# Kernel tuning notes

Hardware: AMD Instinct MI355X
Metric: run time of the kernel (lower is better)

## Reference

```python
import jax, jax.numpy as jnp
import numpy as np
from jax import lax

BIG = 1e30  # finite stand-in for +inf to keep grads NaN-free


def _iso_inc(y):
    """Exact non-decreasing isotonic regression (L2) of a 1-D vector via the
    minimax formula: v_i = max_{j<=i} min_{k>=i} mean(y[j..k]).
    Vectorized O(n^2); equivalent to PAVA."""
    n = y.shape[0]
    csum = jnp.concatenate([jnp.zeros((1,), y.dtype), jnp.cumsum(y)])
    j = jnp.arange(n)[:, None]   # row index (block start)
    k = jnp.arange(n)[None, :]   # col index (block end / position i)
    valid = k >= j
    denom = jnp.where(valid, k - j + 1, 1).astype(y.dtype)
    mean = jnp.where(valid, (csum[k + 1] - csum[j]) / denom, BIG)  # [n, n]
    # A[j, i] = min_{k >= i} mean[j, k]
    A = lax.cummin(mean, axis=1, reverse=True)
    # v_i = max_{j <= i} A[j, i]
    B = jnp.where(j <= k, A, -BIG)
    return jnp.max(B, axis=0)


def _iso_dec(y):
    """Non-increasing isotonic regression (what torchsort's isotonic_l2 solves)."""
    return -_iso_inc(-y)


def _soft_rank_l2(x, strength):
    """torchsort.soft_rank with regularization='l2' (Blondel et al. 2020).
    x: [b, n]; rank along last dim. r = s - iso_dec(s - w) un-permuted,
    where s = sort(x/strength, descending) and w = [n, n-1, ..., 1]."""
    n = x.shape[-1]
    theta = x / strength
    perm = jnp.argsort(-theta, axis=-1)                 # descending sort order
    s = jnp.take_along_axis(theta, perm, axis=-1)
    w = jnp.arange(n, 0, -1).astype(x.dtype)            # [n, n-1, ..., 1]
    iso = jax.vmap(_iso_dec)(s - w)
    ret_sorted = s - iso
    inv = jnp.argsort(perm, axis=-1)                    # inverse permutation
    return jnp.take_along_axis(ret_sorted, inv, axis=-1)


def setup_inputs() -> dict:
    key = jax.random.key(0)
    k1, k2 = jax.random.split(key)
    pred = jax.random.normal(k1, (8, 2048), dtype=jnp.float32)
    target = jax.random.normal(k2, (8, 2048), dtype=jnp.float32)
    return {"pred": pred, "target": target}


def reference(pred, target):
    reg_strength = 1.0
    pred_rank = _soft_rank_l2(pred, reg_strength)
    target_rank = _soft_rank_l2(target, reg_strength)
    pc = pred_rank - pred_rank.mean(axis=-1, keepdims=True)
    tc = target_rank - target_rank.mean(axis=-1, keepdims=True)
    covariance = (pc * tc).sum(axis=-1)
    pred_std = jnp.sqrt((pc ** 2).sum(axis=-1))
    target_std = jnp.sqrt((tc ** 2).sum(axis=-1))
    spearman = covariance / (pred_std * target_std + 1e-8)
    return 1.0 - jnp.mean(spearman)
```

## Files before the change

### kernel.cpp

```cpp
#include <hip/hip_runtime.h>
#include <math.h>

#define N      2048
#define B      8
#define NROW   16
#define CHUNKS 16
#define EPB    128
#define K1T    512
#define K2T    512
#define HALF   256
#define EPT    8

typedef unsigned long long u64;
typedef unsigned int       u32;

#define WS_CORRD_OFF (NROW * N * sizeof(int))

__device__ inline u32 f2key(float f) {
    u32 u = __float_as_uint(f);
    return (u & 0x80000000u) ? ~u : (u | 0x80000000u);
}
__device__ inline double wave_red(double v) {
#pragma unroll
    for (int o = 32; o > 0; o >>= 1) v += __shfl_down(v, o, 64);
    return v;
}

__global__ __launch_bounds__(K1T) void count_pos_kernel(
        const float* __restrict__ pred, const float* __restrict__ target,
        int* __restrict__ posg) {
    __shared__ u64 keys[N];
    __shared__ u32 scnt[K1T];

    const int t  = threadIdx.x;
    const int rr = blockIdx.x >> 4;
    const int ch = blockIdx.x & 15;
    const float* row = (rr < B) ? pred + (size_t)rr * N
                                : target + (size_t)(rr - B) * N;

    {
        const float4 v = *(const float4*)(row + t * 4);
        const int g = t * 4;
        keys[g + 0] = ((u64)f2key(v.x) << 32) | (u32)(g + 0);
        keys[g + 1] = ((u64)f2key(v.y) << 32) | (u32)(g + 1);
        keys[g + 2] = ((u64)f2key(v.z) << 32) | (u32)(g + 2);
        keys[g + 3] = ((u64)f2key(v.w) << 32) | (u32)(g + 3);
    }
    __syncthreads();
    {
        const int e  = t & (EPB - 1);
        const int h  = t >> 7;
        const u64 Ki = keys[ch * EPB + e];
        u32 cnt = 0;
        const int j0 = h * (N / 4);
#pragma unroll 8
        for (int j = j0; j < j0 + N / 4; ++j)
            cnt += (keys[j] > Ki) ? 1u : 0u;
        scnt[t] = cnt;
    }
    __syncthreads();
    if (t < EPB) {
        const u32 p = scnt[t] + scnt[t + 128] + scnt[t + 256] + scnt[t + 384];
        posg[rr * N + ch * EPB + t] = (int)p;
    }
}

__global__ __launch_bounds__(K2T) void pava_rank_corr_kernel(
        const float* __restrict__ pred, const float* __restrict__ target,
        const int* __restrict__ posg, double* __restrict__ corrd) {
    __shared__ float  sv[2][N];
    __shared__ double bsum[2][N];
    __shared__ int    bcnt[2][N];
    __shared__ int    nb[2][HALF];
    __shared__ int    nf_sh[2];
    __shared__ float  rank[2][N];
    __shared__ double redA[8], redB[8], redC[8], redD[8], redE[8];

    const int t  = threadIdx.x;
    const int r  = t >> 8;
    const int tt = t & (HALF - 1);
    const int b  = blockIdx.x;

    const float* row = (r == 0 ? pred : target) + (size_t)b * N;
    const int*   pos = posg + (size_t)(r == 0 ? b : b + B) * N;

    float v8[EPT]; int p8[EPT];
    {
        const int i0 = tt * EPT;
        const float4 va = *(const float4*)(row + i0);
        const float4 vb = *(const float4*)(row + i0 + 4);
        v8[0]=va.x; v8[1]=va.y; v8[2]=va.z; v8[3]=va.w;
        v8[4]=vb.x; v8[5]=vb.y; v8[6]=vb.z; v8[7]=vb.w;
        const int4 pa = *(const int4*)(pos + i0);
        const int4 pb = *(const int4*)(pos + i0 + 4);
        p8[0]=pa.x; p8[1]=pa.y; p8[2]=pa.z; p8[3]=pa.w;
        p8[4]=pb.x; p8[5]=pb.y; p8[6]=pb.z; p8[7]=pb.w;
#pragma unroll
        for (int e = 0; e < EPT; ++e) sv[r][p8[e]] = v8[e];
    }
    __syncthreads();

    {
        const int base = tt * EPT;
        int m = 0;
#pragma unroll
        for (int e = 0; e < EPT; ++e) {
            const int g = base + e;
            double s = (double)sv[r][g] - (double)(N - g);
            int q = 1;
            while (m > 0) {
                const double ps = bsum[r][base + m - 1];
                const int    pq = bcnt[r][base + m - 1];
                if (ps * (double)q < s * (double)pq) { s += ps; q += pq; --m; }
                else break;
            }
            bsum[r][base + m] = s; bcnt[r][base + m] = q; ++m;
        }
        nb[r][tt] = m;
    }

    for (int l = 0; l < 8; ++l) {
        __syncthreads();
        const int pairs = HALF >> (l + 1);
        if (tt < pairs) {
            const int W  = 1 << l;
            const int c  = tt << (l + 1);
            const int lb = c * EPT;
            const int rb = (c + W) * EPT;
            int m = nb[r][c];
            const int rn = nb[r][c + W];
            for (int x = 0; x < rn; ++x) {
                double s = bsum[r][rb + x]; int q = bcnt[r][rb + x];
                while (m > 0) {
                    const double ps = bsum[r][lb + m - 1];
                    const int    pq = bcnt[r][lb + m - 1];
                    if (ps * (double)q < s * (double)pq) { s += ps; q += pq; --m; }
                    else break;
                }
                bsum[r][lb + m] = s; bcnt[r][lb + m] = q; ++m;
            }
            nb[r][c] = m;
        }
    }
    __syncthreads();

    if (tt == 0) {
        const int m = nb[r][0];
        float* bm = (float*)&bsum[r][0];
        int st = 0;
        for (int f = 0; f < m; ++f) {
            const int    cq = bcnt[r][f];
            const double s  = bsum[r][f];
            bcnt[r][f] = st;
            bm[f] = (float)(s / (double)cq);
            st += cq;
        }
        nf_sh[r] = m;
    }
    __syncthreads();

    {
        const int m = nf_sh[r];
        const float* bm = (const float*)&bsum[r][0];
        const int i0 = tt * EPT;
#pragma unroll
        for (int e = 0; e < EPT; ++e) {
            const int p = p8[e];
            int lo = 0, hi = m - 1;
            while (lo < hi) {
                const int mid = (lo + hi + 1) >> 1;
                if (bcnt[r][mid] <= p) lo = mid; else hi = mid - 1;
            }
            rank[r][i0 + e] = v8[e] - bm[lo];
        }
    }
    __syncthreads();

    double sp = 0, st = 0, spp = 0, stt = 0, spt = 0;
    for (int i = t; i < N; i += K2T) {
        const double a = (double)rank[0][i];
        const double c = (double)rank[1][i];
        sp += a; st += c; spp += a * a; stt += c * c; spt += a * c;
    }
    sp  = wave_red(sp);  st  = wave_red(st);
    spp = wave_red(spp); stt = wave_red(stt); spt = wave_red(spt);
    const int w = t >> 6, lane = t & 63;
    if (lane == 0) { redA[w]=sp; redB[w]=st; redC[w]=spp; redD[w]=stt; redE[w]=spt; }
    __syncthreads();
    if (t == 0) {
        double a=0, c=0, aa=0, cc=0, ac=0;
        for (int i = 0; i < 8; ++i) { a+=redA[i]; c+=redB[i]; aa+=redC[i]; cc+=redD[i]; ac+=redE[i]; }
        const double n   = (double)N;
        const double cv  = ac - a * c / n;
        const double vp2 = aa - a * a / n;
        const double vt2 = cc - c * c / n;
        corrd[b] = cv / (sqrt(vp2) * sqrt(vt2) + 1e-8);
    }
}

__global__ void finalize_kernel(const double* __restrict__ corrd,
                                float* __restrict__ out) {
    if (threadIdx.x == 0 && blockIdx.x == 0) {
        double s = 0.0;
        for (int i = 0; i < B; ++i) s += corrd[i];
        out[0] = (float)(1.0 - s / (double)B);
    }
}

extern "C" void kernel_launch(void* const* d_in, const int* in_sizes, int n_in,
                              void* d_out, int out_size, void* d_ws, size_t ws_size,
                              hipStream_t stream) {
    const float* pred   = (const float*)d_in[0];
    const float* target = (const float*)d_in[1];
    float*  out   = (float*)d_out;
    int*    posg  = (int*)d_ws;
    double* corrd = (double*)((char*)d_ws + WS_CORRD_OFF);

    count_pos_kernel<<<NROW * CHUNKS, K1T, 0, stream>>>(pred, target, posg);
    pava_rank_corr_kernel<<<B, K2T, 0, stream>>>(pred, target, posg, corrd);
    finalize_kernel<<<1, 64, 0, stream>>>(corrd, out);
}
```

Baseline: 26.06 us.

## Scatter sorted values in count kernel and fold finalize into atomic add

The counting kernel now writes each element's value to its sorted position in a global buffer and initializes the output to 1. The PAVA kernel reads the presorted values directly instead of doing a shared-memory scatter plus barrier, and it defers the original value and position loads until after the merges. The correlation reduction keeps the pred ranks in registers, and the separate finalize kernel is replaced by a float atomicAdd, removing one kernel launch. This relies on stream ordering for the output initialization, and float atomics make the final summation order nondeterministic.

```diff
diff --git a/kernel.cpp b/kernel.cpp
--- a/kernel.cpp
+++ b/kernel.cpp
@@ -14,12 +14,17 @@
 typedef unsigned long long u64;
 typedef unsigned int       u32;
 
-#define WS_CORRD_OFF (NROW * N * sizeof(int))
+#define WS_POS 0
+#define WS_SV  (NROW * N)
 
 __device__ inline u32 f2key(float f) {
     u32 u = __float_as_uint(f);
     return (u & 0x80000000u) ? ~u : (u | 0x80000000u);
 }
+__device__ inline float key2f(u32 u) {
+    u = (u & 0x80000000u) ? (u & 0x7fffffffu) : ~u;
+    return __uint_as_float(u);
+}
 __device__ inline double wave_red(double v) {
 #pragma unroll
     for (int o = 32; o > 0; o >>= 1) v += __shfl_down(v, o, 64);
@@ -28,7 +33,8 @@
 
 __global__ __launch_bounds__(K1T) void count_pos_kernel(
         const float* __restrict__ pred, const float* __restrict__ target,
-        int* __restrict__ posg) {
+        int* __restrict__ posg, float* __restrict__ svg,
+        float* __restrict__ out) {
     __shared__ u64 keys[N];
     __shared__ u32 scnt[K1T];
 
@@ -37,6 +43,8 @@
     const int ch = blockIdx.x & 15;
     const float* row = (rr < B) ? pred + (size_t)rr * N
                                 : target + (size_t)(rr - B) * N;
+
+    if (blockIdx.x == 0 && t == 0) out[0] = 1.0f;
 
     {
         const float4 v = *(const float4*)(row + t * 4);
@@ -61,60 +69,48 @@
     __syncthreads();
     if (t < EPB) {
         const u32 p = scnt[t] + scnt[t + 128] + scnt[t + 256] + scnt[t + 384];
+        const u64 Ki = keys[ch * EPB + t];
         posg[rr * N + ch * EPB + t] = (int)p;
+        svg[rr * N + (int)p] = key2f((u32)(Ki >> 32));
     }
 }
 
 __global__ __launch_bounds__(K2T) void pava_rank_corr_kernel(
         const float* __restrict__ pred, const float* __restrict__ target,
-        const int* __restrict__ posg, double* __restrict__ corrd) {
-    __shared__ float  sv[2][N];
+        const int* __restrict__ posg, const float* __restrict__ svg,
+        float* __restrict__ out) {
     __shared__ double bsum[2][N];
     __shared__ int    bcnt[2][N];
     __shared__ int    nb[2][HALF];
     __shared__ int    nf_sh[2];
-    __shared__ float  rank[2][N];
-    __shared__ double redA[8], redB[8], redC[8], redD[8], redE[8];
+    __shared__ float  rankt[N];
+    __shared__ double red[5][4];
 
     const int t  = threadIdx.x;
     const int r  = t >> 8;
     const int tt = t & (HALF - 1);
     const int b  = blockIdx.x;
-
-    const float* row = (r == 0 ? pred : target) + (size_t)b * N;
-    const int*   pos = posg + (size_t)(r == 0 ? b : b + B) * N;
-
-    float v8[EPT]; int p8[EPT];
-    {
-        const int i0 = tt * EPT;
-        const float4 va = *(const float4*)(row + i0);
-        const float4 vb = *(const float4*)(row + i0 + 4);
-        v8[0]=va.x; v8[1]=va.y; v8[2]=va.z; v8[3]=va.w;
-        v8[4]=vb.x; v8[5]=vb.y; v8[6]=vb.z; v8[7]=vb.w;
-        const int4 pa = *(const int4*)(pos + i0);
-        const int4 pb = *(const int4*)(pos + i0 + 4);
-        p8[0]=pa.x; p8[1]=pa.y; p8[2]=pa.z; p8[3]=pa.w;
-        p8[4]=pb.x; p8[5]=pb.y; p8[6]=pb.z; p8[7]=pb.w;
-#pragma unroll
-        for (int e = 0; e < EPT; ++e) sv[r][p8[e]] = v8[e];
-    }
-    __syncthreads();
-
-    {
-        const int base = tt * EPT;
+    const int rowid = (r == 0) ? b : b + B;
+    const int i0 = tt * EPT;
+
+    {
+        const float* svrow = svg + (size_t)rowid * N;
+        const float4 sa = *(const float4*)(svrow + i0);
+        const float4 sb = *(const float4*)(svrow + i0 + 4);
+        const float s8[EPT] = {sa.x, sa.y, sa.z, sa.w, sb.x, sb.y, sb.z, sb.w};
         int m = 0;
 #pragma unroll
         for (int e = 0; e < EPT; ++e) {
-            const int g = base + e;
-            double s = (double)sv[r][g] - (double)(N - g);
+            const int g = i0 + e;
+            double s = (double)s8[e] - (double)(N - g);
             int q = 1;
             while (m > 0) {
-                const double ps = bsum[r][base + m - 1];
-                const int    pq = bcnt[r][base + m - 1];
+                const double ps = bsum[r][i0 + m - 1];
+                const int    pq = bcnt[r][i0 + m - 1];
                 if (ps * (double)q < s * (double)pq) { s += ps; q += pq; --m; }
                 else break;
             }
-            bsum[r][base + m] = s; bcnt[r][base + m] = q; ++m;
+            bsum[r][i0 + m] = s; bcnt[r][i0 + m] = q; ++m;
         }
         nb[r][tt] = m;
     }
@@ -159,10 +155,18 @@
     }
     __syncthreads();
 
-    {
+    float r8[EPT];
+    {
+        const float* row = (r == 0 ? pred : target) + (size_t)b * N;
+        const int*   pos = posg + (size_t)rowid * N;
+        const float4 va = *(const float4*)(row + i0);
+        const float4 vb = *(const float4*)(row + i0 + 4);
+        const float v8[EPT] = {va.x, va.y, va.z, va.w, vb.x, vb.y, vb.z, vb.w};
+        const int4 pa = *(const int4*)(pos + i0);
+        const int4 pb = *(const int4*)(pos + i0 + 4);
+        const int p8[EPT] = {pa.x, pa.y, pa.z, pa.w, pb.x, pb.y, pb.z, pb.w};
         const int m = nf_sh[r];
         const float* bm = (const float*)&bsum[r][0];
-        const int i0 = tt * EPT;
 #pragma unroll
         for (int e = 0; e < EPT; ++e) {
             const int p = p8[e];
@@ -171,39 +175,44 @@
                 const int mid = (lo + hi + 1) >> 1;
                 if (bcnt[r][mid] <= p) lo = mid; else hi = mid - 1;
             }
-            rank[r][i0 + e] = v8[e] - bm[lo];
-        }
-    }
-    __syncthreads();
-
-    double sp = 0, st = 0, spp = 0, stt = 0, spt = 0;
-    for (int i = t; i < N; i += K2T) {
-        const double a = (double)rank[0][i];
-        const double c = (double)rank[1][i];
-        sp += a; st += c; spp += a * a; stt += c * c; spt += a * c;
-    }
-    sp  = wave_red(sp);  st  = wave_red(st);
-    spp = wave_red(spp); stt = wave_red(stt); spt = wave_red(spt);
-    const int w = t >> 6, lane = t & 63;
-    if (lane == 0) { redA[w]=sp; redB[w]=st; redC[w]=spp; redD[w]=stt; redE[w]=spt; }
+            r8[e] = v8[e] - bm[lo];
+        }
+    }
+    if (r == 1) {
+#pragma unroll
+        for (int e = 0; e < EPT; ++e) rankt[i0 + e] = r8[e];
+    }
+    __syncthreads();
+
+    if (r == 0) {
+        double sp = 0, st = 0, spp = 0, stt = 0, spt = 0;
+#pragma unroll
+        for (int e = 0; e < EPT; ++e) {
+            const double a = (double)r8[e];
+            const double c = (double)rankt[i0 + e];
+            sp += a; st += c; spp += a * a; stt += c * c; spt += a * c;
+        }
+        sp  = wave_red(sp);  st  = wave_red(st);
+        spp = wave_red(spp); stt = wave_red(stt); spt = wave_red(spt);
+        const int w = t >> 6, lane = t & 63;
+        if (lane == 0) {
+            red[0][w] = sp; red[1][w] = st; red[2][w] = spp;
+            red[3][w] = stt; red[4][w] = spt;
+        }
+    }
     __syncthreads();
     if (t == 0) {
-        double a=0, c=0, aa=0, cc=0, ac=0;
-        for (int i = 0; i < 8; ++i) { a+=redA[i]; c+=redB[i]; aa+=redC[i]; cc+=redD[i]; ac+=redE[i]; }
+        double a = 0, c = 0, aa = 0, cc = 0, ac = 0;
+        for (int i = 0; i < 4; ++i) {
+            a += red[0][i]; c += red[1][i]; aa += red[2][i];
+            cc += red[3][i]; ac += red[4][i];
+        }
         const double n   = (double)N;
         const double cv  = ac - a * c / n;
         const double vp2 = aa - a * a / n;
         const double vt2 = cc - c * c / n;
-        corrd[b] = cv / (sqrt(vp2) * sqrt(vt2) + 1e-8);
-    }
-}
-
-__global__ void finalize_kernel(const double* __restrict__ corrd,
-                                float* __restrict__ out) {
-    if (threadIdx.x == 0 && blockIdx.x == 0) {
-        double s = 0.0;
-        for (int i = 0; i < B; ++i) s += corrd[i];
-        out[0] = (float)(1.0 - s / (double)B);
+        const double corr = cv / (sqrt(vp2) * sqrt(vt2) + 1e-8);
+        atomicAdd(out, (float)(-corr / (double)B));
     }
 }
 
@@ -212,11 +221,10 @@
                               hipStream_t stream) {
     const float* pred   = (const float*)d_in[0];
     const float* target = (const float*)d_in[1];
-    float*  out   = (float*)d_out;
-    int*    posg  = (int*)d_ws;
-    double* corrd = (double*)((char*)d_ws + WS_CORRD_OFF);
-
-    count_pos_kernel<<<NROW * CHUNKS, K1T, 0, stream>>>(pred, target, posg);
-    pava_rank_corr_kernel<<<B, K2T, 0, stream>>>(pred, target, posg, corrd);
-    finalize_kernel<<<1, 64, 0, stream>>>(corrd, out);
-}
+    float* out  = (float*)d_out;
+    int*   posg = (int*)d_ws + WS_POS;
+    float* svg  = (float*)d_ws + WS_SV;
+
+    count_pos_kernel<<<NROW * CHUNKS, K1T, 0, stream>>>(pred, target, posg, svg, out);
+    pava_rank_corr_kernel<<<B, K2T, 0, stream>>>(pred, target, posg, svg, out);
+}
```

Result: faster. 23.47 us (-9.9%).
